# Performance work log

Hardware: AMD Instinct MI355X
Metric: run time of the kernel (lower is better)

The kernel has to match this reference:

```python
import jax, jax.numpy as jnp
import numpy as np

N = 50000
E = 640000
R = 8


def setup_inputs() -> dict:
    key = jax.random.key(0)
    ks = jax.random.split(key, 12)
    in_c, hid_c, out_c = 128, 128, 64
    s1 = 1.0 / np.sqrt(in_c)
    s2 = 1.0 / np.sqrt(hid_c)
    s3 = 1.0 / np.sqrt(out_c)
    return {
        "x": jax.random.normal(ks[0], (N, in_c), dtype=jnp.float32),
        "edge_index": jax.random.randint(ks[1], (2, E), 0, N),
        "edge_type": jax.random.randint(ks[2], (E,), 0, R),
        # layer 1: per-relation weights, root weight, bias
        "W1": jax.random.uniform(ks[3], (R, in_c, hid_c), minval=-s1, maxval=s1, dtype=jnp.float32),
        "root1": jax.random.uniform(ks[4], (in_c, hid_c), minval=-s1, maxval=s1, dtype=jnp.float32),
        "b1": jnp.zeros((hid_c,), dtype=jnp.float32),
        # layer 2
        "W2": jax.random.uniform(ks[5], (R, hid_c, out_c), minval=-s2, maxval=s2, dtype=jnp.float32),
        "root2": jax.random.uniform(ks[6], (hid_c, out_c), minval=-s2, maxval=s2, dtype=jnp.float32),
        "b2": jnp.zeros((out_c,), dtype=jnp.float32),
        # classifier
        "Wc": jax.random.uniform(ks[7], (out_c, 2), minval=-s3, maxval=s3, dtype=jnp.float32),
        "bc": jnp.zeros((2,), dtype=jnp.float32),
    }


def _rgcn_layer(x, edge_index, edge_type, W, root, b):
    # PyG RGCNConv with aggr='mean': per relation r, mean-aggregate source
    # features over edges of type r into destinations, then apply W_r.
    # out = sum_r mean_agg_r(x) @ W_r + x @ root + b
    src, dst = edge_index[0], edge_index[1]
    msgs = x[src]  # [E, Fin] gather
    seg = edge_type * N + dst  # combined (relation, dst) segment id
    sums = jax.ops.segment_sum(msgs, seg, num_segments=R * N)  # [R*N, Fin]
    cnt = jax.ops.segment_sum(jnp.ones((msgs.shape[0],), x.dtype), seg, num_segments=R * N)
    mean = sums / jnp.maximum(cnt, 1.0)[:, None]  # zero-degree -> 0
    mean = mean.reshape(R, N, x.shape[1])  # [R, N, Fin]
    out = jnp.einsum("rnf,rfo->no", mean, W) + x @ root + b
    return out


def reference(x, edge_index, edge_type, W1, root1, b1, W2, root2, b2, Wc, bc):
    h = jax.nn.relu(_rgcn_layer(x, edge_index, edge_type, W1, root1, b1))
    # dropout (p=0.3) is identity in eval mode
    h = jax.nn.relu(_rgcn_layer(h, edge_index, edge_type, W2, root2, b2))
    logits = h @ Wc + bc  # [N, 2]
    return logits
```

## Files before the change

### kernel.cpp

```cpp
#include <hip/hip_runtime.h>

#define NN 50000
#define EE 640000
#define RR 8
#define CAP 64

typedef __bf16 bf16x8 __attribute__((ext_vector_type(8)));
typedef float  f32x4  __attribute__((ext_vector_type(4)));
typedef const __attribute__((address_space(1))) unsigned int* gas_p;
typedef __attribute__((address_space(3))) unsigned int* las_p;

__device__ __forceinline__ unsigned short f2b(float f) {
  unsigned int u = __float_as_uint(f);
  u += 0x7fffu + ((u >> 16) & 1u);
  return (unsigned short)(u >> 16);
}
__device__ __forceinline__ float b2f(unsigned short h) {
  return __uint_as_float(((unsigned int)h) << 16);
}

__global__ void k_f32_to_bf16_x4(const float* __restrict__ src,
                                 unsigned short* __restrict__ dst, int n4) {
  int t = blockIdx.x * blockDim.x + threadIdx.x;
  if (t >= n4) return;
  float4 v = reinterpret_cast<const float4*>(src)[t];
  ushort4 o = make_ushort4(f2b(v.x), f2b(v.y), f2b(v.z), f2b(v.w));
  reinterpret_cast<ushort4*>(dst)[t] = o;
}

__global__ void k_build_b1(const float* __restrict__ W1, const float* __restrict__ root1,
                           unsigned short* __restrict__ B1T) {
  int t = blockIdx.x * 256 + threadIdx.x;
  if (t >= 1152 * 128) return;
  int j = t >> 7, k = t & 127;
  float v = (j < 1024) ? W1[((j >> 7) << 14) + (k << 7) + (j & 127)]
                       : root1[(k << 7) + (j - 1024)];
  B1T[t] = f2b(v);
}

__global__ void k_build_b2(const float* __restrict__ W2, const float* __restrict__ root2,
                           unsigned short* __restrict__ B2T) {
  int t = blockIdx.x * 256 + threadIdx.x;
  if (t >= 640 * 128) return;
  int j = t >> 7, k = t & 127;
  float v = 0.0f;
  if (j < 512)      v = W2[((j >> 6) << 13) + (k << 6) + (j & 63)];
  else if (j < 576) v = root2[(k << 6) + (j - 512)];
  B2T[t] = f2b(v);
}

__global__ void k_edges(const int* __restrict__ src, const int* __restrict__ dst,
                        const int* __restrict__ typ,
                        int* __restrict__ cursor, unsigned int* __restrict__ entries) {
  int e = blockIdx.x * 256 + threadIdx.x;
  if (e >= EE) return;
  int d = dst[e], r = typ[e];
  int pos = atomicAdd(&cursor[d], 1);
  if (pos < CAP)
    entries[d * CAP + pos] = (unsigned int)src[e] | ((unsigned int)r << 16);
}

__global__ __launch_bounds__(256, 2) void k_gemm(
    const unsigned short* __restrict__ A, const unsigned short* __restrict__ BT,
    unsigned short* __restrict__ Y, float* __restrict__ rootOut,
    const float* __restrict__ bias, int M, int nsplit, int nroot) {
  __shared__ __align__(16) unsigned short As[128 * 128];
  __shared__ __align__(16) unsigned short Bs[128 * 128];
  const int tid = threadIdx.x;
  const int m0 = blockIdx.x * 128;
  const int n0 = blockIdx.y * 128;
  const int wv = tid >> 6;
  const int ln = tid & 63;

  {
    unsigned short* Lbuf = (wv < 2) ? As : Bs;
    const unsigned short* Gbuf = (wv < 2) ? (A + (size_t)m0 * 128) : (BT + (size_t)n0 * 128);
    const int rbase = (wv & 1) * 64;
#pragma unroll
    for (int c = 0; c < 16; ++c) {
      int r = rbase + c * 4 + (ln >> 4);
      int c16 = ln & 15;
      int j = c16 ^ (r & 15);
      const unsigned short* gp = Gbuf + (size_t)r * 128 + j * 8;
      unsigned short* lp = Lbuf + r * 128 + c16 * 8;
      __builtin_amdgcn_global_load_lds((gas_p)(const void*)gp, (las_p)(void*)lp, 16, 0, 0);
    }
  }
  __syncthreads();

  const int lane = tid & 63;
  const int wave = tid >> 6;
  const int wm = (wave >> 1) << 6;
  const int wn = (wave & 1) << 6;
  const int l15 = lane & 15;
  const int quad = lane >> 4;
  f32x4 acc[4][4] = {};
#pragma unroll
  for (int kk = 0; kk < 4; ++kk) {
    const int sw = ((kk * 4 + quad) ^ l15) * 8;
    bf16x8 af[4], bfr[4];
#pragma unroll
    for (int i = 0; i < 4; ++i) {
      af[i]  = *reinterpret_cast<const bf16x8*>(&As[(wm + i * 16 + l15) * 128 + sw]);
      bfr[i] = *reinterpret_cast<const bf16x8*>(&Bs[(wn + i * 16 + l15) * 128 + sw]);
    }
#pragma unroll
    for (int i = 0; i < 4; ++i)
#pragma unroll
      for (int j = 0; j < 4; ++j)
        acc[i][j] = __builtin_amdgcn_mfma_f32_16x16x32_bf16(bfr[j], af[i], acc[i][j], 0, 0, 0);
  }

  if (n0 >= nsplit) {
#pragma unroll
    for (int i = 0; i < 4; ++i) {
      const int m = wm + i * 16 + l15;
      if (m0 + m >= M) continue;
#pragma unroll
      for (int j = 0; j < 4; ++j) {
        const int col = n0 + wn + j * 16 + quad * 4 - nsplit;
        if (col < nroot) {
          float4 b4 = *reinterpret_cast<const float4*>(&bias[col]);
          float4 v = make_float4(acc[i][j][0] + b4.x, acc[i][j][1] + b4.y,
                                 acc[i][j][2] + b4.z, acc[i][j][3] + b4.w);
          *reinterpret_cast<float4*>(&rootOut[(size_t)(m0 + m) * nroot + col]) = v;
        }
      }
    }
  } else {
    __syncthreads();
    unsigned short* Cs = As;
#pragma unroll
    for (int i = 0; i < 4; ++i) {
      const int m = wm + i * 16 + l15;
#pragma unroll
      for (int j = 0; j < 4; ++j) {
        const int c8 = ((wn + j * 16) >> 2) + quad;
        const int c8s = c8 ^ (l15 << 1);
        uint2 pk;
        pk.x = (unsigned int)f2b(acc[i][j][0]) | ((unsigned int)f2b(acc[i][j][1]) << 16);
        pk.y = (unsigned int)f2b(acc[i][j][2]) | ((unsigned int)f2b(acc[i][j][3]) << 16);
        *reinterpret_cast<uint2*>(&Cs[m * 128 + c8s * 4]) = pk;
      }
    }
    __syncthreads();
#pragma unroll
    for (int it = 0; it < 8; ++it) {
      const int L = tid + it * 256;
      const int m = L >> 4;
      const int c16 = L & 15;
      const int c16s = c16 ^ (m & 15);
      if (m0 + m < M) {
        uint4 v = *reinterpret_cast<const uint4*>(&Cs[m * 128 + c16s * 8]);
        *reinterpret_cast<uint4*>(&Y[(size_t)(m0 + m) * nsplit + n0 + c16 * 8]) = v;
      }
    }
  }
}

__global__ void k_agg1(const unsigned int* __restrict__ entries,
                       const int* __restrict__ cursor,
                       const unsigned short* __restrict__ y,
                       const float* __restrict__ hpre,
                       unsigned int* __restrict__ hbf) {
  const int d = blockIdx.x * 4 + (threadIdx.x >> 6);
  const int lane = threadIdx.x & 63;
  int deg = cursor[d];
  if (deg > CAP) deg = CAP;
  unsigned int e = (lane < deg) ? entries[d * CAP + lane] : 0u;
  const int myr = (e >> 16) & 7;
  float sc = 0.f;
#pragma unroll
  for (int r = 0; r < 8; ++r) {
    unsigned long long bm = __ballot(lane < deg && myr == r);
    if (myr == r) sc = __builtin_amdgcn_rcpf((float)__popcll(bm));
  }
  if (lane >= deg) sc = 0.f;

  const int g = lane >> 4;
  const int l16 = lane & 15;
  float a[8] = {};
  const int T = (deg + 7) >> 3;
  for (int t = 0; t < T; ++t) {
    const int i0 = t * 8 + g;
    const int i1 = i0 + 4;
    unsigned int e0 = __shfl(e, i0, 64);  float s0 = __shfl(sc, i0, 64);
    unsigned int e1 = __shfl(e, i1, 64);  float s1 = __shfl(sc, i1, 64);
    uint4 pk0 = *reinterpret_cast<const uint4*>(
        y + (((size_t)(e0 & 0xffffu)) << 10) + (((e0 >> 16) & 7u) << 7) + (l16 << 3));
    uint4 pk1 = *reinterpret_cast<const uint4*>(
        y + (((size_t)(e1 & 0xffffu)) << 10) + (((e1 >> 16) & 7u) << 7) + (l16 << 3));
    a[0] += b2f((unsigned short)pk0.x) * s0;
    a[1] += __uint_as_float(pk0.x & 0xffff0000u) * s0;
    a[2] += b2f((unsigned short)pk0.y) * s0;
    a[3] += __uint_as_float(pk0.y & 0xffff0000u) * s0;
    a[4] += b2f((unsigned short)pk0.z) * s0;
    a[5] += __uint_as_float(pk0.z & 0xffff0000u) * s0;
    a[6] += b2f((unsigned short)pk0.w) * s0;
    a[7] += __uint_as_float(pk0.w & 0xffff0000u) * s0;
    a[0] += b2f((unsigned short)pk1.x) * s1;
    a[1] += __uint_as_float(pk1.x & 0xffff0000u) * s1;
    a[2] += b2f((unsigned short)pk1.y) * s1;
    a[3] += __uint_as_float(pk1.y & 0xffff0000u) * s1;
    a[4] += b2f((unsigned short)pk1.z) * s1;
    a[5] += __uint_as_float(pk1.z & 0xffff0000u) * s1;
    a[6] += b2f((unsigned short)pk1.w) * s1;
    a[7] += __uint_as_float(pk1.w & 0xffff0000u) * s1;
  }
#pragma unroll
  for (int j = 0; j < 8; ++j) {
    a[j] += __shfl_xor(a[j], 16, 64);
    a[j] += __shfl_xor(a[j], 32, 64);
  }
  if (g == 0) {
    const float4* hp = reinterpret_cast<const float4*>(hpre) + (size_t)d * 32 + l16 * 2;
    float4 h0 = hp[0];
    float4 h1 = hp[1];
    float v0 = fmaxf(a[0] + h0.x, 0.f), v1 = fmaxf(a[1] + h0.y, 0.f);
    float v2 = fmaxf(a[2] + h0.z, 0.f), v3 = fmaxf(a[3] + h0.w, 0.f);
    float v4 = fmaxf(a[4] + h1.x, 0.f), v5 = fmaxf(a[5] + h1.y, 0.f);
    float v6 = fmaxf(a[6] + h1.z, 0.f), v7 = fmaxf(a[7] + h1.w, 0.f);
    uint4 o;
    o.x = (unsigned int)f2b(v0) | ((unsigned int)f2b(v1) << 16);
    o.y = (unsigned int)f2b(v2) | ((unsigned int)f2b(v3) << 16);
    o.z = (unsigned int)f2b(v4) | ((unsigned int)f2b(v5) << 16);
    o.w = (unsigned int)f2b(v6) | ((unsigned int)f2b(v7) << 16);
    reinterpret_cast<uint4*>(hbf)[(size_t)d * 16 + l16] = o;
  }
}

__global__ void k_agg2(const unsigned int* __restrict__ entries,
                       const int* __restrict__ cursor,
                       const unsigned short* __restrict__ y,
                       const float* __restrict__ hpre,
                       const float* __restrict__ Wc, const float* __restrict__ bc,
                       float* __restrict__ out) {
  const int d = blockIdx.x * 4 + (threadIdx.x >> 6);
  const int lane = threadIdx.x & 63;
  int deg = cursor[d];
  if (deg > CAP) deg = CAP;
  unsigned int e = (lane < deg) ? entries[d * CAP + lane] : 0u;
  const int myr = (e >> 16) & 7;
  float sc = 0.f;
#pragma unroll
  for (int r = 0; r < 8; ++r) {
    unsigned long long bm = __ballot(lane < deg && myr == r);
    if (myr == r) sc = __builtin_amdgcn_rcpf((float)__popcll(bm));
  }
  if (lane >= deg) sc = 0.f;

  const int g = lane >> 3;
  const int l8 = lane & 7;
  float a[8] = {};
  const int T = (deg + 15) >> 4;
  for (int t = 0; t < T; ++t) {
    const int i0 = t * 16 + g;
    const int i1 = i0 + 8;
    unsigned int e0 = __shfl(e, i0, 64);  float s0 = __shfl(sc, i0, 64);
    unsigned int e1 = __shfl(e, i1, 64);  float s1 = __shfl(sc, i1, 64);
    uint4 pk0 = *reinterpret_cast<const uint4*>(
        y + (((size_t)(e0 & 0xffffu)) << 9) + (((e0 >> 16) & 7u) << 6) + (l8 << 3));
    uint4 pk1 = *reinterpret_cast<const uint4*>(
        y + (((size_t)(e1 & 0xffffu)) << 9) + (((e1 >> 16) & 7u) << 6) + (l8 << 3));
    a[0] += b2f((unsigned short)pk0.x) * s0;
    a[1] += __uint_as_float(pk0.x & 0xffff0000u) * s0;
    a[2] += b2f((unsigned short)pk0.y) * s0;
    a[3] += __uint_as_float(pk0.y & 0xffff0000u) * s0;
    a[4] += b2f((unsigned short)pk0.z) * s0;
    a[5] += __uint_as_float(pk0.z & 0xffff0000u) * s0;
    a[6] += b2f((unsigned short)pk0.w) * s0;
    a[7] += __uint_as_float(pk0.w & 0xffff0000u) * s0;
    a[0] += b2f((unsigned short)pk1.x) * s1;
    a[1] += __uint_as_float(pk1.x & 0xffff0000u) * s1;
    a[2] += b2f((unsigned short)pk1.y) * s1;
    a[3] += __uint_as_float(pk1.y & 0xffff0000u) * s1;
    a[4] += b2f((unsigned short)pk1.z) * s1;
    a[5] += __uint_as_float(pk1.z & 0xffff0000u) * s1;
    a[6] += b2f((unsigned short)pk1.w) * s1;
    a[7] += __uint_as_float(pk1.w & 0xffff0000u) * s1;
  }
#pragma unroll
  for (int j = 0; j < 8; ++j) {
    a[j] += __shfl_xor(a[j], 8, 64);
    a[j] += __shfl_xor(a[j], 16, 64);
    a[j] += __shfl_xor(a[j], 32, 64);
  }
  const float4* hp = reinterpret_cast<const float4*>(hpre) + (size_t)d * 16 + l8 * 2;
  float4 h0 = hp[0];
  float4 h1 = hp[1];
  float v0 = fmaxf(a[0] + h0.x, 0.f), v1 = fmaxf(a[1] + h0.y, 0.f);
  float v2 = fmaxf(a[2] + h0.z, 0.f), v3 = fmaxf(a[3] + h0.w, 0.f);
  float v4 = fmaxf(a[4] + h1.x, 0.f), v5 = fmaxf(a[5] + h1.y, 0.f);
  float v6 = fmaxf(a[6] + h1.z, 0.f), v7 = fmaxf(a[7] + h1.w, 0.f);
  const float4* wc4 = reinterpret_cast<const float4*>(Wc) + l8 * 4;
  float4 w0 = wc4[0], w1 = wc4[1], w2 = wc4[2], w3 = wc4[3];
  float p0 = v0 * w0.x + v1 * w0.z + v2 * w1.x + v3 * w1.z
           + v4 * w2.x + v5 * w2.z + v6 * w3.x + v7 * w3.z;
  float p1 = v0 * w0.y + v1 * w0.w + v2 * w1.y + v3 * w1.w
           + v4 * w2.y + v5 * w2.w + v6 * w3.y + v7 * w3.w;
  p0 += __shfl_xor(p0, 1, 64); p1 += __shfl_xor(p1, 1, 64);
  p0 += __shfl_xor(p0, 2, 64); p1 += __shfl_xor(p1, 2, 64);
  p0 += __shfl_xor(p0, 4, 64); p1 += __shfl_xor(p1, 4, 64);
  if (lane == 0) {
    out[d * 2 + 0] = p0 + bc[0];
    out[d * 2 + 1] = p1 + bc[1];
  }
}

extern "C" void kernel_launch(void* const* d_in, const int* in_sizes, int n_in,
                              void* d_out, int out_size, void* d_ws, size_t ws_size,
                              hipStream_t stream) {
  const float* x     = (const float*)d_in[0];
  const int*   ei    = (const int*)d_in[1];
  const int*   et    = (const int*)d_in[2];
  const float* W1    = (const float*)d_in[3];
  const float* root1 = (const float*)d_in[4];
  const float* b1    = (const float*)d_in[5];
  const float* W2    = (const float*)d_in[6];
  const float* root2 = (const float*)d_in[7];
  const float* b2    = (const float*)d_in[8];
  const float* Wc    = (const float*)d_in[9];
  const float* bc    = (const float*)d_in[10];
  const int* srcI = ei;
  const int* dstI = ei + EE;

  char* ws = (char*)d_ws;
  unsigned short* xb      = (unsigned short*)(ws);
  unsigned int*   hbf     = (unsigned int*)(ws);
  unsigned short* B1T     = (unsigned short*)(ws + 12800000);
  unsigned short* B2T     = (unsigned short*)(ws + 13094912);
  int*            cursor  = (int*)(ws + 13258752);
  unsigned int*   entries = (unsigned int*)(ws + 13458752);
  float*          hpre    = (float*)(ws + 26258752);
  unsigned short* y1      = (unsigned short*)(ws + 51858752);
  unsigned short* y2      = y1;

  hipMemsetAsync(cursor, 0, 200000, stream);
  k_f32_to_bf16_x4<<<(1600000 + 255) / 256, 256, 0, stream>>>(x, xb, 1600000);
  k_build_b1<<<(1152 * 128 + 255) / 256, 256, 0, stream>>>(W1, root1, B1T);
  k_build_b2<<<(640 * 128 + 255) / 256, 256, 0, stream>>>(W2, root2, B2T);
  k_edges<<<(EE + 255) / 256, 256, 0, stream>>>(srcI, dstI, et, cursor, entries);

  k_gemm<<<dim3(391, 9), 256, 0, stream>>>(xb, B1T, y1, hpre, b1, NN, 1024, 128);
  k_agg1<<<NN / 4, 256, 0, stream>>>(entries, cursor, y1, hpre, hbf);

  k_gemm<<<dim3(391, 5), 256, 0, stream>>>((const unsigned short*)hbf, B2T, y2, hpre, b2, NN, 512, 64);
  k_agg2<<<NN / 4, 256, 0, stream>>>(entries, cursor, y2, hpre, Wc, bc, (float*)d_out);
}
```

Before: 276.1 us.

## Reuse A tile across multiple double-buffered B sub-tiles in GEMM

Each GEMM block now loads its 128-row A tile once, then loops over several 64-column B sub-tiles. The next B sub-tile is prefetched into a second LDS buffer while the current one is computed. This cuts repeated A loads by reducing the grid's column dimension, at the cost of fewer blocks and less parallelism. The LDS-staged coalesced epilogue is replaced with direct 8-byte bf16 stores to global memory, which may give less efficient write coalescing.

New measurement: 290.9 us. 1.05x slower.

```diff
diff --git a/kernel.cpp b/kernel.cpp
--- a/kernel.cpp
+++ b/kernel.cpp
@@ -63,27 +63,32 @@
 __global__ __launch_bounds__(256, 2) void k_gemm(
     const unsigned short* __restrict__ A, const unsigned short* __restrict__ BT,
     unsigned short* __restrict__ Y, float* __restrict__ rootOut,
-    const float* __restrict__ bias, int M, int nsplit, int nroot) {
+    const float* __restrict__ bias, int M, int nsplit, int nroot, int nsub) {
   __shared__ __align__(16) unsigned short As[128 * 128];
-  __shared__ __align__(16) unsigned short Bs[128 * 128];
+  __shared__ __align__(16) unsigned short Bs[2][64 * 128];
   const int tid = threadIdx.x;
   const int m0 = blockIdx.x * 128;
-  const int n0 = blockIdx.y * 128;
-  const int wv = tid >> 6;
-  const int ln = tid & 63;
+  const int n0g = blockIdx.y * nsub * 64;
 
   {
-    unsigned short* Lbuf = (wv < 2) ? As : Bs;
-    const unsigned short* Gbuf = (wv < 2) ? (A + (size_t)m0 * 128) : (BT + (size_t)n0 * 128);
-    const int rbase = (wv & 1) * 64;
-#pragma unroll
-    for (int c = 0; c < 16; ++c) {
-      int r = rbase + c * 4 + (ln >> 4);
-      int c16 = ln & 15;
+#pragma unroll
+    for (int c = 0; c < 8; ++c) {
+      int L = tid + c * 256;
+      int r = L >> 4, c16 = L & 15;
       int j = c16 ^ (r & 15);
-      const unsigned short* gp = Gbuf + (size_t)r * 128 + j * 8;
-      unsigned short* lp = Lbuf + r * 128 + c16 * 8;
-      __builtin_amdgcn_global_load_lds((gas_p)(const void*)gp, (las_p)(void*)lp, 16, 0, 0);
+      __builtin_amdgcn_global_load_lds(
+          (gas_p)(const void*)(A + (size_t)(m0 + r) * 128 + j * 8),
+          (las_p)(void*)(As + r * 128 + c16 * 8), 16, 0, 0);
+    }
+    const unsigned short* Gb = BT + (size_t)n0g * 128;
+#pragma unroll
+    for (int c = 0; c < 4; ++c) {
+      int L = tid + c * 256;
+      int r = L >> 4, c16 = L & 15;
+      int j = c16 ^ (r & 15);
+      __builtin_amdgcn_global_load_lds(
+          (gas_p)(const void*)(Gb + (size_t)r * 128 + j * 8),
+          (las_p)(void*)(Bs[0] + r * 128 + c16 * 8), 16, 0, 0);
     }
   }
   __syncthreads();
@@ -91,70 +96,79 @@
   const int lane = tid & 63;
   const int wave = tid >> 6;
   const int wm = (wave >> 1) << 6;
-  const int wn = (wave & 1) << 6;
+  const int wn = (wave & 1) << 5;
   const int l15 = lane & 15;
   const int quad = lane >> 4;
-  f32x4 acc[4][4] = {};
-#pragma unroll
-  for (int kk = 0; kk < 4; ++kk) {
-    const int sw = ((kk * 4 + quad) ^ l15) * 8;
-    bf16x8 af[4], bfr[4];
-#pragma unroll
-    for (int i = 0; i < 4; ++i) {
-      af[i]  = *reinterpret_cast<const bf16x8*>(&As[(wm + i * 16 + l15) * 128 + sw]);
-      bfr[i] = *reinterpret_cast<const bf16x8*>(&Bs[(wn + i * 16 + l15) * 128 + sw]);
-    }
-#pragma unroll
-    for (int i = 0; i < 4; ++i)
-#pragma unroll
-      for (int j = 0; j < 4; ++j)
-        acc[i][j] = __builtin_amdgcn_mfma_f32_16x16x32_bf16(bfr[j], af[i], acc[i][j], 0, 0, 0);
-  }
-
-  if (n0 >= nsplit) {
-#pragma unroll
-    for (int i = 0; i < 4; ++i) {
-      const int m = wm + i * 16 + l15;
-      if (m0 + m >= M) continue;
-#pragma unroll
-      for (int j = 0; j < 4; ++j) {
-        const int col = n0 + wn + j * 16 + quad * 4 - nsplit;
-        if (col < nroot) {
-          float4 b4 = *reinterpret_cast<const float4*>(&bias[col]);
-          float4 v = make_float4(acc[i][j][0] + b4.x, acc[i][j][1] + b4.y,
-                                 acc[i][j][2] + b4.z, acc[i][j][3] + b4.w);
-          *reinterpret_cast<float4*>(&rootOut[(size_t)(m0 + m) * nroot + col]) = v;
+
+  int buf = 0;
+  for (int s = 0; s < nsub; ++s) {
+    if (s + 1 < nsub) {
+      const unsigned short* Gb = BT + (size_t)(n0g + (s + 1) * 64) * 128;
+      unsigned short* Lb = Bs[buf ^ 1];
+#pragma unroll
+      for (int c = 0; c < 4; ++c) {
+        int L = tid + c * 256;
+        int r = L >> 4, c16 = L & 15;
+        int j = c16 ^ (r & 15);
+        __builtin_amdgcn_global_load_lds(
+            (gas_p)(const void*)(Gb + (size_t)r * 128 + j * 8),
+            (las_p)(void*)(Lb + r * 128 + c16 * 8), 16, 0, 0);
+      }
+    }
+
+    f32x4 acc[4][2] = {};
+    const unsigned short* Bc = Bs[buf];
+#pragma unroll
+    for (int kk = 0; kk < 4; ++kk) {
+      const int sw = ((kk * 4 + quad) ^ l15) * 8;
+      bf16x8 af[4], bfr[2];
+#pragma unroll
+      for (int i = 0; i < 4; ++i)
+        af[i] = *reinterpret_cast<const bf16x8*>(&As[(wm + i * 16 + l15) * 128 + sw]);
+#pragma unroll
+      for (int j = 0; j < 2; ++j)
+        bfr[j] = *reinterpret_cast<const bf16x8*>(&Bc[(wn + j * 16 + l15) * 128 + sw]);
+#pragma unroll
+      for (int i = 0; i < 4; ++i)
+#pragma unroll
+        for (int j = 0; j < 2; ++j)
+          acc[i][j] = __builtin_amdgcn_mfma_f32_16x16x32_bf16(bfr[j], af[i], acc[i][j], 0, 0, 0);
+    }
+    __syncthreads();
+
+    const int scol = n0g + s * 64;
+    if (scol >= nsplit) {
+#pragma unroll
+      for (int i = 0; i < 4; ++i) {
+        const int m = wm + i * 16 + l15;
+        if (m0 + m >= M) continue;
+#pragma unroll
+        for (int j = 0; j < 2; ++j) {
+          const int col = scol + wn + j * 16 + quad * 4 - nsplit;
+          if (col < nroot) {
+            float4 b4 = *reinterpret_cast<const float4*>(&bias[col]);
+            float4 v = make_float4(acc[i][j][0] + b4.x, acc[i][j][1] + b4.y,
+                                   acc[i][j][2] + b4.z, acc[i][j][3] + b4.w);
+            *reinterpret_cast<float4*>(&rootOut[(size_t)(m0 + m) * nroot + col]) = v;
+          }
         }
       }
-    }
-  } else {
-    __syncthreads();
-    unsigned short* Cs = As;
-#pragma unroll
-    for (int i = 0; i < 4; ++i) {
-      const int m = wm + i * 16 + l15;
-#pragma unroll
-      for (int j = 0; j < 4; ++j) {
-        const int c8 = ((wn + j * 16) >> 2) + quad;
-        const int c8s = c8 ^ (l15 << 1);
-        uint2 pk;
-        pk.x = (unsigned int)f2b(acc[i][j][0]) | ((unsigned int)f2b(acc[i][j][1]) << 16);
-        pk.y = (unsigned int)f2b(acc[i][j][2]) | ((unsigned int)f2b(acc[i][j][3]) << 16);
-        *reinterpret_cast<uint2*>(&Cs[m * 128 + c8s * 4]) = pk;
+    } else {
+#pragma unroll
+      for (int i = 0; i < 4; ++i) {
+        const int m = wm + i * 16 + l15;
+        if (m0 + m >= M) continue;
+        unsigned short* yp = Y + (size_t)(m0 + m) * nsplit + scol + wn + quad * 4;
+#pragma unroll
+        for (int j = 0; j < 2; ++j) {
+          uint2 pk;
+          pk.x = (unsigned int)f2b(acc[i][j][0]) | ((unsigned int)f2b(acc[i][j][1]) << 16);
+          pk.y = (unsigned int)f2b(acc[i][j][2]) | ((unsigned int)f2b(acc[i][j][3]) << 16);
+          *reinterpret_cast<uint2*>(yp + j * 16) = pk;
+        }
       }
     }
-    __syncthreads();
-#pragma unroll
-    for (int it = 0; it < 8; ++it) {
-      const int L = tid + it * 256;
-      const int m = L >> 4;
-      const int c16 = L & 15;
-      const int c16s = c16 ^ (m & 15);
-      if (m0 + m < M) {
-        uint4 v = *reinterpret_cast<const uint4*>(&Cs[m * 128 + c16s * 8]);
-        *reinterpret_cast<uint4*>(&Y[(size_t)(m0 + m) * nsplit + n0 + c16 * 8]) = v;
-      }
-    }
+    buf ^= 1;
   }
 }
 
@@ -341,9 +355,9 @@
   k_build_b2<<<(640 * 128 + 255) / 256, 256, 0, stream>>>(W2, root2, B2T);
   k_edges<<<(EE + 255) / 256, 256, 0, stream>>>(srcI, dstI, et, cursor, entries);
 
-  k_gemm<<<dim3(391, 9), 256, 0, stream>>>(xb, B1T, y1, hpre, b1, NN, 1024, 128);
+  k_gemm<<<dim3(391, 3), 256, 0, stream>>>(xb, B1T, y1, hpre, b1, NN, 1024, 128, 6);
   k_agg1<<<NN / 4, 256, 0, stream>>>(entries, cursor, y1, hpre, hbf);
 
-  k_gemm<<<dim3(391, 5), 256, 0, stream>>>((const unsigned short*)hbf, B2T, y2, hpre, b2, NN, 512, 64);
+  k_gemm<<<dim3(391, 2), 256, 0, stream>>>((const unsigned short*)hbf, B2T, y2, hpre, b2, NN, 512, 64, 5);
   k_agg2<<<NN / 4, 256, 0, stream>>>(entries, cursor, y2, hpre, Wc, bc, (float*)d_out);
 }
```
